# Optimization experiments

Hardware: AMD Instinct MI355X
Metric: run time of the kernel (lower is better)

## Reference

```python
import jax, jax.numpy as jnp
import numpy as np

HIDDEN = 2048
NUM_Q_HEADS = 32
NUM_KV_HEADS = 8
HEAD_DIM = HIDDEN // NUM_Q_HEADS  # 64
GROUPS = NUM_Q_HEADS // NUM_KV_HEADS  # 4
MAX_WAVELENGTH = 10000.0
B, S = 2, 1024
NEG_INF = -1e9  # keras Softmax masking constant


def apply_rope(x, start_index=0, max_wavelength=MAX_WAVELENGTH):
    # x: [b, s, h, d]; keras_hub RotaryEmbedding (split-half / Llama style)
    d = x.shape[-1]
    s = x.shape[1]
    freq_range = jnp.arange(0, d, 2, dtype=jnp.float32)
    inverse_freq = 1.0 / (max_wavelength ** (freq_range / d))  # [d/2]
    positions = jnp.arange(s, dtype=jnp.float32) + start_index
    freq = positions[:, None] * inverse_freq[None, :]  # [s, d/2]
    emb = jnp.concatenate([freq, freq], axis=-1)[None, :, None, :]  # [1,s,1,d]
    cos = jnp.cos(emb).astype(x.dtype)
    sin = jnp.sin(emb).astype(x.dtype)
    x1, x2 = jnp.split(x, 2, axis=-1)
    half_rot = jnp.concatenate([-x2, x1], axis=-1)
    return x * cos + half_rot * sin


def setup_inputs() -> dict:
    key = jax.random.key(0)
    k1, k2, k3, k4, k5 = jax.random.split(key, 5)
    hidden_states = jax.random.normal(k1, (B, S, HIDDEN), dtype=jnp.float32)
    # causal mask, broadcast over batch
    attention_mask = jnp.broadcast_to(
        jnp.tril(jnp.ones((S, S), dtype=bool))[None], (B, S, S)
    )
    scale = 1.0 / np.sqrt(HIDDEN)
    Wq = jax.random.normal(k2, (HIDDEN, NUM_Q_HEADS * HEAD_DIM), dtype=jnp.float32) * scale
    Wk = jax.random.normal(k3, (HIDDEN, NUM_KV_HEADS * HEAD_DIM), dtype=jnp.float32) * scale
    Wv = jax.random.normal(k4, (HIDDEN, NUM_KV_HEADS * HEAD_DIM), dtype=jnp.float32) * scale
    Wo = jax.random.normal(k5, (NUM_Q_HEADS * HEAD_DIM, HIDDEN), dtype=jnp.float32) * scale
    return {"hidden_states": hidden_states, "attention_mask": attention_mask,
            "Wq": Wq, "Wk": Wk, "Wv": Wv, "Wo": Wo}


def reference(hidden_states, attention_mask, Wq, Wk, Wv, Wo):
    b, s, _ = hidden_states.shape
    q = (hidden_states @ Wq).reshape(b, s, NUM_Q_HEADS, HEAD_DIM)
    k = (hidden_states @ Wk).reshape(b, s, NUM_KV_HEADS, HEAD_DIM)
    v = (hidden_states @ Wv).reshape(b, s, NUM_KV_HEADS, HEAD_DIM)
    q = apply_rope(q)
    k = apply_rope(k)
    # GQA: repeat kv heads to match query heads (ops.repeat on axis 2)
    k = jnp.repeat(k, GROUPS, axis=2)
    v = jnp.repeat(v, GROUPS, axis=2)
    inv_norm = 1.0 / np.sqrt(HEAD_DIM)
    scores = jnp.einsum("bquh,bkuh->buqk", q, k) * inv_norm  # [b, h, q, k]
    scores = scores.astype(jnp.float32)
    scores = jnp.where(attention_mask[:, None, :, :], scores, NEG_INF)
    probs = jax.nn.softmax(scores, axis=-1).astype(hidden_states.dtype)
    attn = jnp.einsum("buqk,bkuh->bquh", probs, v)  # [b, q, h, hd]
    attn = attn.reshape(b, s, HIDDEN)
    return attn @ Wo
```

## Files before the change

kernel.cpp:

```cpp
#include <hip/hip_runtime.h>
#include <hip/hip_bf16.h>
#include <math.h>

#define S_LEN 1024
#define BATCH 2
#define HIDDEN 2048
#define NQH 32
#define NKVH 8
#define HD 64
#define LDQKV 3072
#define M_ROWS (BATCH * S_LEN)

typedef __attribute__((ext_vector_type(8))) short bf16x8;
typedef __attribute__((ext_vector_type(4))) float f32x4;

typedef unsigned int uint32_g __attribute__((address_space(1)));
typedef unsigned int uint32_l __attribute__((address_space(3)));

static __device__ __forceinline__ void load_lds16(const void* g, void* l) {
    __builtin_amdgcn_global_load_lds((const uint32_g*)g, (uint32_l*)l, 16, 0, 0);
}

static __device__ __forceinline__ short f2bf(float f) {
    union { __hip_bfloat16 h; short s; } cv;
    cv.h = __float2bfloat16(f);
    return cv.s;
}

__global__ __launch_bounds__(256) void conv_all_kernel(
    const float* __restrict__ X,
    const float* __restrict__ Wq, const float* __restrict__ Wk,
    const float* __restrict__ Wv, const float* __restrict__ Wo,
    short* __restrict__ Xb, short* __restrict__ Wqkvt, short* __restrict__ Wot,
    float2* __restrict__ cs2)
{
    __shared__ short Ts[64][68];
    const int tid = threadIdx.x;

    if (blockIdx.z == 4) {
        int flat = blockIdx.y * 32 + blockIdx.x;
        size_t base = (size_t)flat * 4096 + (size_t)tid * 16;
        #pragma unroll
        for (int rep = 0; rep < 2; ++rep) {
            size_t i = base + rep * 8;
            float4 a = *reinterpret_cast<const float4*>(X + i);
            float4 b = *reinterpret_cast<const float4*>(X + i + 4);
            union { bf16x8 v; short s[8]; } t;
            t.s[0] = f2bf(a.x); t.s[1] = f2bf(a.y); t.s[2] = f2bf(a.z); t.s[3] = f2bf(a.w);
            t.s[4] = f2bf(b.x); t.s[5] = f2bf(b.y); t.s[6] = f2bf(b.z); t.s[7] = f2bf(b.w);
            *reinterpret_cast<bf16x8*>(Xb + i) = t.v;
        }
        if (flat < 128) {
            int g = flat * 256 + tid;
            int s = g >> 5, i = g & 31;
            float inv_freq = 1.0f / powf(10000.0f, (float)i / 32.0f);
            float freq = (float)s * inv_freq;
            double sn, cs;
            sincos((double)freq, &sn, &cs);
            cs2[g] = make_float2((float)cs, (float)sn);
        }
        return;
    }

    const float* src; short* dst; int N;
    switch (blockIdx.z) {
        case 0: src = Wq; dst = Wqkvt;                         N = 2048; break;
        case 1: src = Wk; dst = Wqkvt + (size_t)2048 * 2048;   N = 512;  break;
        case 2: src = Wv; dst = Wqkvt + (size_t)2560 * 2048;   N = 512;  break;
        default: src = Wo; dst = Wot;                          N = 2048; break;
    }
    const int n0 = blockIdx.x * 64, k0 = blockIdx.y * 64;
    if (n0 >= N) return;

    #pragma unroll
    for (int rep = 0; rep < 4; ++rep) {
        int idx = rep * 256 + tid;
        int row = idx >> 4, c4 = (idx & 15) * 4;
        float4 v = *reinterpret_cast<const float4*>(
            src + (size_t)(k0 + row) * N + n0 + c4);
        ushort4 u;
        u.x = (unsigned short)f2bf(v.x); u.y = (unsigned short)f2bf(v.y);
        u.z = (unsigned short)f2bf(v.z); u.w = (unsigned short)f2bf(v.w);
        *reinterpret_cast<ushort4*>(&Ts[row][c4]) = u;
    }
    __syncthreads();
    #pragma unroll
    for (int rep = 0; rep < 2; ++rep) {
        int idx = rep * 256 + tid;
        int n = idx >> 3, kc = (idx & 7) * 8;
        union { bf16x8 v; short s[8]; } t;
        #pragma unroll
        for (int j = 0; j < 8; ++j) t.s[j] = Ts[kc + j][n];
        *reinterpret_cast<bf16x8*>(dst + (size_t)(n0 + n) * 2048 + k0 + kc) = t.v;
    }
}

template <bool ROPE_BF16>
__global__ __launch_bounds__(256) void gemm_bf16_kernel(
    const short* __restrict__ A, const short* __restrict__ Bt,
    float* __restrict__ C, short* __restrict__ Cb,
    short* __restrict__ vt_g,
    const float2* __restrict__ cs2, int K, int ldc)
{
    const int n0 = blockIdx.x * 64, m0 = blockIdx.y * 128;
    const int tid = threadIdx.x;
    const int w = tid >> 6, lane = tid & 63;
    const int m15 = lane & 15, q4 = lane >> 4;

    __shared__ short SL[128 * 64 + 64 * 64];
    short (*As)[64] = (short(*)[64])SL;
    short (*Bs)[64] = (short(*)[64])(SL + 128 * 64);

    f32x4 acc[2][4];
    #pragma unroll
    for (int i = 0; i < 2; ++i)
        #pragma unroll
        for (int j = 0; j < 4; ++j) acc[i][j] = (f32x4){0.f, 0.f, 0.f, 0.f};

    const int srow = lane >> 3;
    const int pchunk = lane & 7;

    for (int k0 = 0; k0 < K; k0 += 64) {
        __syncthreads();
        #pragma unroll
        for (int r = 0; r < 4; ++r) {
            int row = (w * 4 + r) * 8 + srow;
            int lchunk = pchunk ^ (row & 7);
            load_lds16(A + (size_t)(m0 + row) * K + k0 + lchunk * 8,
                       &As[(w * 4 + r) * 8][0]);
        }
        #pragma unroll
        for (int r = 0; r < 2; ++r) {
            int row = (w * 2 + r) * 8 + srow;
            int lchunk = pchunk ^ (row & 7);
            load_lds16(Bt + (size_t)(n0 + row) * K + k0 + lchunk * 8,
                       &Bs[(w * 2 + r) * 8][0]);
        }
        __syncthreads();

        #pragma unroll
        for (int ch = 0; ch < 2; ++ch) {
            bf16x8 af[2], bf[4];
            #pragma unroll
            for (int mt = 0; mt < 2; ++mt) {
                int row = w * 32 + mt * 16 + m15;
                af[mt] = *reinterpret_cast<const bf16x8*>(
                    &As[row][(((ch * 4 + q4) ^ (row & 7))) * 8]);
            }
            #pragma unroll
            for (int nt = 0; nt < 4; ++nt) {
                int row = nt * 16 + m15;
                bf[nt] = *reinterpret_cast<const bf16x8*>(
                    &Bs[row][(((ch * 4 + q4) ^ (row & 7))) * 8]);
            }
            #pragma unroll
            for (int mt = 0; mt < 2; ++mt)
                #pragma unroll
                for (int nt = 0; nt < 4; ++nt)
                    acc[mt][nt] = __builtin_amdgcn_mfma_f32_16x16x32_bf16(
                        af[mt], bf[nt], acc[mt][nt], 0, 0, 0);
        }
    }

    if (!ROPE_BF16) {
        #pragma unroll
        for (int mt = 0; mt < 2; ++mt)
            #pragma unroll
            for (int nt = 0; nt < 4; ++nt)
                #pragma unroll
                for (int reg = 0; reg < 4; ++reg)
                    C[(size_t)(m0 + w * 32 + mt * 16 + q4 * 4 + reg) * ldc
                      + n0 + nt * 16 + m15] = acc[mt][nt][reg];
    } else if (n0 < 2560) {
        #pragma unroll
        for (int mt = 0; mt < 2; ++mt) {
            #pragma unroll
            for (int reg = 0; reg < 4; ++reg) {
                int row = m0 + w * 32 + mt * 16 + q4 * 4 + reg;
                int s = row & (S_LEN - 1);
                float2 t0 = cs2[s * 32 + m15];
                float2 t1 = cs2[s * 32 + 16 + m15];
                float a0 = acc[mt][0][reg], a1 = acc[mt][1][reg];
                float a2 = acc[mt][2][reg], a3 = acc[mt][3][reg];
                size_t base = (size_t)row * ldc + n0 + m15;
                Cb[base +  0] = f2bf(a0 * t0.x - a2 * t0.y);
                Cb[base + 16] = f2bf(a1 * t1.x - a3 * t1.y);
                Cb[base + 32] = f2bf(a2 * t0.x + a0 * t0.y);
                Cb[base + 48] = f2bf(a3 * t1.x + a1 * t1.y);
            }
        }
    } else {
        __syncthreads();
        short (*VT)[136] = (short(*)[136])SL;
        #pragma unroll
        for (int mt = 0; mt < 2; ++mt) {
            #pragma unroll
            for (int nt = 0; nt < 4; ++nt) {
                ushort4 u;
                u.x = (unsigned short)f2bf(acc[mt][nt][0]);
                u.y = (unsigned short)f2bf(acc[mt][nt][1]);
                u.z = (unsigned short)f2bf(acc[mt][nt][2]);
                u.w = (unsigned short)f2bf(acc[mt][nt][3]);
                *reinterpret_cast<ushort4*>(
                    &VT[nt * 16 + m15][w * 32 + mt * 16 + q4 * 4]) = u;
            }
        }
        __syncthreads();
        const int kvh = (n0 - 2560) >> 6;
        const int b = m0 >> 10, k0loc = m0 & (S_LEN - 1);
        const int dim = tid >> 2, kc = (tid & 3) * 32;
        short* dst = vt_g + (size_t)((b * 8 + kvh) * 64 + dim) * S_LEN + k0loc + kc;
        #pragma unroll
        for (int u = 0; u < 4; ++u)
            *reinterpret_cast<bf16x8*>(dst + u * 8) =
                *reinterpret_cast<const bf16x8*>(&VT[dim][kc + u * 8]);
    }
}

__global__ __launch_bounds__(512) void attn_kernel(
    const short* __restrict__ qkvb, const short* __restrict__ vt_g,
    short* __restrict__ attn_b)
{
    const int qt = 7 - blockIdx.x;
    const int h  = blockIdx.y;
    const int b  = blockIdx.z;
    const int tid = threadIdx.x;
    const int w = tid >> 6, lane = tid & 63;
    const int kvh = h >> 2;
    const int m15 = lane & 15, q4 = lane >> 4;

    __shared__ short Ks[64][72];
    __shared__ short Vt[64][72];
    __shared__ float Ps[8][16][68];

    const int rowbase = qt * 128 + w * 16;
    const bf16x8 qf0 = *reinterpret_cast<const bf16x8*>(
        qkvb + (size_t)(b * S_LEN + rowbase + m15) * LDQKV + h * HD + q4 * 8);
    const bf16x8 qf1 = *reinterpret_cast<const bf16x8*>(
        qkvb + (size_t)(b * S_LEN + rowbase + m15) * LDQKV + h * HD + 32 + q4 * 8);

    f32x4 o4[4];
    #pragma unroll
    for (int i = 0; i < 4; ++i) o4[i] = (f32x4){0.f, 0.f, 0.f, 0.f};
    float lsum[4] = {0.f, 0.f, 0.f, 0.f};

    const int ntiles = qt * 2 + 2;
    const int j8 = tid >> 3, c8 = (tid & 7) * 8;
    const short* kbase = qkvb + (size_t)(b * S_LEN) * LDQKV + 2048 + kvh * HD;
    const short* vbase = vt_g + (size_t)((b * 8 + kvh) * 64 + j8) * S_LEN;

    for (int t = 0; t < ntiles; ++t) {
        __syncthreads();
        *reinterpret_cast<bf16x8*>(&Ks[j8][c8]) =
            *reinterpret_cast<const bf16x8*>(kbase + (size_t)(t * 64 + j8) * LDQKV + c8);
        *reinterpret_cast<bf16x8*>(&Vt[j8][c8]) =
            *reinterpret_cast<const bf16x8*>(vbase + t * 64 + c8);
        __syncthreads();

        #pragma unroll
        for (int nt = 0; nt < 4; ++nt) {
            f32x4 acc = (f32x4){0.f, 0.f, 0.f, 0.f};
            bf16x8 kf0 = *reinterpret_cast<const bf16x8*>(&Ks[nt * 16 + m15][q4 * 8]);
            bf16x8 kf1 = *reinterpret_cast<const bf16x8*>(&Ks[nt * 16 + m15][32 + q4 * 8]);
            acc = __builtin_amdgcn_mfma_f32_16x16x32_bf16(qf0, kf0, acc, 0, 0, 0);
            acc = __builtin_amdgcn_mfma_f32_16x16x32_bf16(qf1, kf1, acc, 0, 0, 0);
            int colg = t * 64 + nt * 16 + m15;
            #pragma unroll
            for (int reg = 0; reg < 4; ++reg) {
                int rowg = rowbase + q4 * 4 + reg;
                float sc = acc[reg] * 0.125f;
                float p = (colg <= rowg) ? __expf(fminf(sc, 60.f)) : 0.f;
                lsum[reg] += p;
                Ps[w][q4 * 4 + reg][nt * 16 + m15] = p;
            }
        }

        bf16x8 pf[2];
        #pragma unroll
        for (int ch = 0; ch < 2; ++ch) {
            f32x4 pa = *reinterpret_cast<const f32x4*>(&Ps[w][m15][ch * 32 + q4 * 8]);
            f32x4 pb = *reinterpret_cast<const f32x4*>(&Ps[w][m15][ch * 32 + q4 * 8 + 4]);
            union { bf16x8 v; short s[8]; } tb;
            tb.s[0] = f2bf(pa[0]); tb.s[1] = f2bf(pa[1]);
            tb.s[2] = f2bf(pa[2]); tb.s[3] = f2bf(pa[3]);
            tb.s[4] = f2bf(pb[0]); tb.s[5] = f2bf(pb[1]);
            tb.s[6] = f2bf(pb[2]); tb.s[7] = f2bf(pb[3]);
            pf[ch] = tb.v;
        }

        #pragma unroll
        for (int nt2 = 0; nt2 < 4; ++nt2) {
            bf16x8 vf0 = *reinterpret_cast<const bf16x8*>(&Vt[nt2 * 16 + m15][q4 * 8]);
            bf16x8 vf1 = *reinterpret_cast<const bf16x8*>(&Vt[nt2 * 16 + m15][32 + q4 * 8]);
            o4[nt2] = __builtin_amdgcn_mfma_f32_16x16x32_bf16(pf[0], vf0, o4[nt2], 0, 0, 0);
            o4[nt2] = __builtin_amdgcn_mfma_f32_16x16x32_bf16(pf[1], vf1, o4[nt2], 0, 0, 0);
        }
    }

    float invl[4];
    #pragma unroll
    for (int reg = 0; reg < 4; ++reg) {
        float l = lsum[reg];
        l += __shfl_xor(l, 1, 64);
        l += __shfl_xor(l, 2, 64);
        l += __shfl_xor(l, 4, 64);
        l += __shfl_xor(l, 8, 64);
        invl[reg] = 1.0f / l;
    }

    #pragma unroll
    for (int nt2 = 0; nt2 < 4; ++nt2)
        #pragma unroll
        for (int reg = 0; reg < 4; ++reg)
            attn_b[(size_t)(b * S_LEN + rowbase + q4 * 4 + reg) * HIDDEN
                   + h * HD + nt2 * 16 + m15] = f2bf(o4[nt2][reg] * invl[reg]);
}

extern "C" void kernel_launch(void* const* d_in, const int* in_sizes, int n_in,
                              void* d_out, int out_size, void* d_ws, size_t ws_size,
                              hipStream_t stream) {
    const float* X  = (const float*)d_in[0];
    const float* Wq = (const float*)d_in[2];
    const float* Wk = (const float*)d_in[3];
    const float* Wv = (const float*)d_in[4];
    const float* Wo = (const float*)d_in[5];
    float* out = (float*)d_out;

    short*  qkvb  = (short*)d_ws;
    short*  Xb    = qkvb + (size_t)M_ROWS * LDQKV;
    short*  Wqkvt = Xb + (size_t)HIDDEN * HIDDEN;
    short*  Wot   = Wqkvt + (size_t)LDQKV * HIDDEN;
    short*  vt_g  = Wot + (size_t)HIDDEN * HIDDEN;
    float2* cs2   = (float2*)(vt_g + (size_t)16 * 64 * S_LEN);
    short*  attn_b = Xb;

    conv_all_kernel<<<dim3(32, 32, 5), dim3(256), 0, stream>>>(
        X, Wq, Wk, Wv, Wo, Xb, Wqkvt, Wot, cs2);

    gemm_bf16_kernel<true><<<dim3(48, 16), dim3(256), 0, stream>>>(
        Xb, Wqkvt, nullptr, qkvb, vt_g, cs2, 2048, LDQKV);
    attn_kernel<<<dim3(8, 32, 2), dim3(512), 0, stream>>>(qkvb, vt_g, attn_b);
    gemm_bf16_kernel<false><<<dim3(32, 16), dim3(256), 0, stream>>>(
        attn_b, Wot, out, nullptr, nullptr, nullptr, 2048, HIDDEN);
}
```

Measured before the change: 212.3 us.

## Shrink attention query tile to 64 rows with async swizzled LDS K/V loads

The attention kernel moves from 128-row query tiles with 512 threads to 64-row tiles with 256 threads, doubling the grid. Causal work per block now follows 64-row granularity, so the diagonal blocks waste less masked compute and more blocks are available to fill the GPU. K and V tiles are loaded straight into LDS with global_load_lds using an XOR swizzle in place of padding, which removes the register round trip and is meant to avoid bank conflicts. The softmax exponent uses exp2f with a folded log2e scale. Each K/V tile is now reused by fewer query rows, so global K/V traffic rises.

```diff
diff --git a/kernel.cpp b/kernel.cpp
--- a/kernel.cpp
+++ b/kernel.cpp
@@ -217,11 +217,11 @@
     }
 }
 
-__global__ __launch_bounds__(512) void attn_kernel(
+__global__ __launch_bounds__(256) void attn_kernel(
     const short* __restrict__ qkvb, const short* __restrict__ vt_g,
     short* __restrict__ attn_b)
 {
-    const int qt = 7 - blockIdx.x;
+    const int qt = 15 - blockIdx.x;
     const int h  = blockIdx.y;
     const int b  = blockIdx.z;
     const int tid = threadIdx.x;
@@ -229,11 +229,11 @@
     const int kvh = h >> 2;
     const int m15 = lane & 15, q4 = lane >> 4;
 
-    __shared__ short Ks[64][72];
-    __shared__ short Vt[64][72];
-    __shared__ float Ps[8][16][68];
-
-    const int rowbase = qt * 128 + w * 16;
+    __shared__ short Ks[64][64];
+    __shared__ short Vt[64][64];
+    __shared__ float Ps[4][16][68];
+
+    const int rowbase = qt * 64 + w * 16;
     const bf16x8 qf0 = *reinterpret_cast<const bf16x8*>(
         qkvb + (size_t)(b * S_LEN + rowbase + m15) * LDQKV + h * HD + q4 * 8);
     const bf16x8 qf1 = *reinterpret_cast<const bf16x8*>(
@@ -244,32 +244,39 @@
     for (int i = 0; i < 4; ++i) o4[i] = (f32x4){0.f, 0.f, 0.f, 0.f};
     float lsum[4] = {0.f, 0.f, 0.f, 0.f};
 
-    const int ntiles = qt * 2 + 2;
-    const int j8 = tid >> 3, c8 = (tid & 7) * 8;
+    const int ntiles = qt + 1;
+    const int r8 = lane >> 3, p8 = lane & 7;
+    const int lch = (p8 ^ r8) * 8;
     const short* kbase = qkvb + (size_t)(b * S_LEN) * LDQKV + 2048 + kvh * HD;
-    const short* vbase = vt_g + (size_t)((b * 8 + kvh) * 64 + j8) * S_LEN;
+    const short* vbase = vt_g + (size_t)(b * 8 + kvh) * 64 * S_LEN;
 
     for (int t = 0; t < ntiles; ++t) {
         __syncthreads();
-        *reinterpret_cast<bf16x8*>(&Ks[j8][c8]) =
-            *reinterpret_cast<const bf16x8*>(kbase + (size_t)(t * 64 + j8) * LDQKV + c8);
-        *reinterpret_cast<bf16x8*>(&Vt[j8][c8]) =
-            *reinterpret_cast<const bf16x8*>(vbase + t * 64 + c8);
-        __syncthreads();
-
+        {
+            int row0 = w * 16 + r8, row1 = w * 16 + 8 + r8;
+            load_lds16(kbase + (size_t)(t * 64 + row0) * LDQKV + lch, &Ks[w * 16][0]);
+            load_lds16(kbase + (size_t)(t * 64 + row1) * LDQKV + lch, &Ks[w * 16 + 8][0]);
+            load_lds16(vbase + (size_t)row0 * S_LEN + t * 64 + lch, &Vt[w * 16][0]);
+            load_lds16(vbase + (size_t)row1 * S_LEN + t * 64 + lch, &Vt[w * 16 + 8][0]);
+        }
+        __syncthreads();
+
+        const int xr = m15 & 7;
         #pragma unroll
         for (int nt = 0; nt < 4; ++nt) {
             f32x4 acc = (f32x4){0.f, 0.f, 0.f, 0.f};
-            bf16x8 kf0 = *reinterpret_cast<const bf16x8*>(&Ks[nt * 16 + m15][q4 * 8]);
-            bf16x8 kf1 = *reinterpret_cast<const bf16x8*>(&Ks[nt * 16 + m15][32 + q4 * 8]);
+            bf16x8 kf0 = *reinterpret_cast<const bf16x8*>(
+                &Ks[nt * 16 + m15][(q4 ^ xr) * 8]);
+            bf16x8 kf1 = *reinterpret_cast<const bf16x8*>(
+                &Ks[nt * 16 + m15][((4 + q4) ^ xr) * 8]);
             acc = __builtin_amdgcn_mfma_f32_16x16x32_bf16(qf0, kf0, acc, 0, 0, 0);
             acc = __builtin_amdgcn_mfma_f32_16x16x32_bf16(qf1, kf1, acc, 0, 0, 0);
             int colg = t * 64 + nt * 16 + m15;
             #pragma unroll
             for (int reg = 0; reg < 4; ++reg) {
                 int rowg = rowbase + q4 * 4 + reg;
-                float sc = acc[reg] * 0.125f;
-                float p = (colg <= rowg) ? __expf(fminf(sc, 60.f)) : 0.f;
+                float p = (colg <= rowg)
+                    ? exp2f(fminf(acc[reg] * 0.180336880f, 80.f)) : 0.f;
                 lsum[reg] += p;
                 Ps[w][q4 * 4 + reg][nt * 16 + m15] = p;
             }
@@ -290,8 +297,10 @@
 
         #pragma unroll
         for (int nt2 = 0; nt2 < 4; ++nt2) {
-            bf16x8 vf0 = *reinterpret_cast<const bf16x8*>(&Vt[nt2 * 16 + m15][q4 * 8]);
-            bf16x8 vf1 = *reinterpret_cast<const bf16x8*>(&Vt[nt2 * 16 + m15][32 + q4 * 8]);
+            bf16x8 vf0 = *reinterpret_cast<const bf16x8*>(
+                &Vt[nt2 * 16 + m15][(q4 ^ xr) * 8]);
+            bf16x8 vf1 = *reinterpret_cast<const bf16x8*>(
+                &Vt[nt2 * 16 + m15][((4 + q4) ^ xr) * 8]);
             o4[nt2] = __builtin_amdgcn_mfma_f32_16x16x32_bf16(pf[0], vf0, o4[nt2], 0, 0, 0);
             o4[nt2] = __builtin_amdgcn_mfma_f32_16x16x32_bf16(pf[1], vf1, o4[nt2], 0, 0, 0);
         }
@@ -339,7 +348,7 @@
 
     gemm_bf16_kernel<true><<<dim3(48, 16), dim3(256), 0, stream>>>(
         Xb, Wqkvt, nullptr, qkvb, vt_g, cs2, 2048, LDQKV);
-    attn_kernel<<<dim3(8, 32, 2), dim3(512), 0, stream>>>(qkvb, vt_g, attn_b);
+    attn_kernel<<<dim3(16, 32, 2), dim3(256), 0, stream>>>(qkvb, vt_g, attn_b);
     gemm_bf16_kernel<false><<<dim3(32, 16), dim3(256), 0, stream>>>(
         attn_b, Wot, out, nullptr, nullptr, nullptr, 2048, HIDDEN);
 }
```

Result: no change. 212.2 us (-0.0%).
